# Kernel optimization log

Measured on AMD Instinct MI355X. Metric: run time of the kernel, lower is better.

Reference implementation:

```python
import jax, jax.numpy as jnp
import numpy as np

N = 50000   # nodes
E = 800000  # edges
IN = 128    # input_channels
HID = 256   # hidden_channels
G = 64      # graphs
R = 3       # num_relations
META = 38
EPS = 1e-5


def _glorot(key, shape):
    fan_in, fan_out = shape[-2], shape[-1]
    lim = np.sqrt(6.0 / (fan_in + fan_out)).astype(np.float32)
    return jax.random.uniform(key, shape, jnp.float32, -lim, lim)


def setup_inputs() -> dict:
    key = jax.random.key(0)
    ks = iter(jax.random.split(key, 40))
    inp = {}
    inp["x"] = jax.random.normal(next(ks), (N, IN), jnp.float32)
    inp["edge_attr"] = jax.random.normal(next(ks), (E, 1), jnp.float32)  # unused by module
    inp["edge_index"] = jax.random.randint(next(ks), (2, E), 0, N)
    inp["edge_type"] = jax.random.randint(next(ks), (E,), 0, R)
    inp["MetaData"] = jax.random.normal(next(ks), (G, META), jnp.float32)
    inp["batch"] = jnp.sort(jax.random.randint(next(ks), (N,), 0, G))
    dims = [(IN, 100), (100, HID), (HID, HID), (HID, HID)]
    for l, (din, dout) in enumerate(dims):
        inp[f"W{l}"] = _glorot(next(ks), (R, din, dout))      # per-relation weights
        inp[f"R{l}"] = _glorot(next(ks), (din, dout))          # root weight
        inp[f"b{l}"] = jnp.zeros((dout,), jnp.float32)         # conv bias
        inp[f"g{l}"] = jnp.ones((dout,), jnp.float32)          # BN gamma
        inp[f"bb{l}"] = jnp.zeros((dout,), jnp.float32)        # BN beta
    inp["lin1_w"] = _glorot(next(ks), (HID + META, 100))
    inp["lin1_b"] = jnp.zeros((100,), jnp.float32)
    inp["lin2_w"] = _glorot(next(ks), (100, 1))
    inp["lin2_b"] = jnp.zeros((1,), jnp.float32)
    return inp


def reference(x, edge_attr, edge_index, edge_type, MetaData, batch,
              W0, R0, b0, g0, bb0, W1, R1, b1, g1, bb1,
              W2, R2, b2, g2, bb2, W3, R3, b3, g3, bb3,
              lin1_w, lin1_b, lin2_w, lin2_b):
    src, dst = edge_index[0], edge_index[1]
    seg = edge_type * N + dst  # combined (relation, dst) segment id
    ones_e = jnp.ones((E,), x.dtype)
    cnt = jax.ops.segment_sum(ones_e, seg, num_segments=R * N).reshape(R, N, 1)
    cnt = jnp.maximum(cnt, 1.0)

    def conv(h, W, Rw, b):
        # per-relation transform then gather-scatter mean aggregation (PyG RGCNConv, aggr='mean')
        H = jnp.einsum('ni,rio->rno', h, W)          # [R,N,out]
        msg = H[edge_type, src]                       # [E,out]
        agg = jax.ops.segment_sum(msg, seg, num_segments=R * N)
        agg = agg.reshape(R, N, -1) / cnt
        return agg.sum(0) + h @ Rw + b

    def bn(h, g, bb):  # training-mode BatchNorm1d over nodes
        mu = h.mean(0)
        var = h.var(0)
        return (h - mu) * jax.lax.rsqrt(var + EPS) * g + bb

    for W, Rw, b, g, bb in [(W0, R0, b0, g0, bb0), (W1, R1, b1, g1, bb1),
                            (W2, R2, b2, g2, bb2), (W3, R3, b3, g3, bb3)]:
        x = bn(conv(x, W, Rw, b), g, bb)

    # global_mean_pool
    sums = jax.ops.segment_sum(x, batch, num_segments=G)
    cnts = jax.ops.segment_sum(jnp.ones((N, 1), x.dtype), batch, num_segments=G)
    xg = sums / jnp.maximum(cnts, 1.0)

    h = jnp.concatenate([xg, MetaData], axis=1) @ lin1_w + lin1_b
    # dropout p=0.5 is identity in eval mode
    return h @ lin2_w + lin2_b
```

## Files before the change

kernel.cpp:

```cpp
#include <hip/hip_runtime.h>
#include <hip/hip_bf16.h>

#define NN 50000
#define EE 800000
#define GG 64
#define RR 3
#define METAD 38
#define NSEG (RR*NN)
#define EPSV 1e-5f

typedef __bf16 bf_t;
typedef __attribute__((ext_vector_type(8))) __bf16 bf16x8;
typedef __attribute__((ext_vector_type(4))) __bf16 bf16x4;
typedef __attribute__((ext_vector_type(2))) __bf16 bf16x2;
typedef __attribute__((ext_vector_type(4))) float f32x4;
typedef __attribute__((address_space(1))) void gas_t;
typedef __attribute__((address_space(3))) void las_t;

__device__ __forceinline__ float loadf(const void* p, size_t i, int flag){
  return flag ? ((const float*)p)[i] : (float)(((const bf_t*)p)[i]);
}

__global__ __launch_bounds__(256) void detect_kernel(const void* __restrict__ xraw,
                                                     int* __restrict__ flag){
  __shared__ int found;
  if (threadIdx.x == 0) found = 0;
  __syncthreads();
  const unsigned short* u = (const unsigned short*)xraw;
  for (int i = threadIdx.x; i < 65536; i += 256){
    int e = (u[i] >> 7) & 0xFF;
    if (e >= 0xF0) found = 1;
  }
  __syncthreads();
  if (threadIdx.x == 0) *flag = found;
}

struct CvtJobs {
  const void* src[17];
  float* dst[17];
  int n[17];
};

__global__ __launch_bounds__(256) void cvt_many(CvtJobs j, const int* __restrict__ flag){
  int job = blockIdx.y;
  int i = blockIdx.x*256 + threadIdx.x;
  if (i < j.n[job]) j.dst[job][i] = loadf(j.src[job], i, *flag);
}

__global__ __launch_bounds__(256) void pack_w(const void* __restrict__ W,
                                              const void* __restrict__ R,
                                              bf_t* __restrict__ out,
                                              int D, int O, int dplog,
                                              const int* __restrict__ flag){
  int id = blockIdx.x*256 + threadIdx.x;
  int DP4 = 1 << (dplog + 2);
  int o = id >> (dplog + 2);
  int k = id & (DP4 - 1);
  int r = k >> dplog;
  int i = k & ((1 << dplog) - 1);
  float v = 0.f;
  int fl = *flag;
  if (i < D && o < O){
    if (r < 3) v = loadf(W, ((size_t)r*D + i)*O + o, fl);
    else       v = loadf(R, (size_t)i*O + o, fl);
  }
  out[(size_t)o*DP4 + k] = (bf_t)v;
}

__global__ __launch_bounds__(256) void counti_kernel(const int* __restrict__ ei,
                                                     const int* __restrict__ et,
                                                     int* __restrict__ cnt){
  int e = blockIdx.x*256 + threadIdx.x;
  if (e < EE) atomicAdd(&cnt[et[e]*NN + ei[EE + e]], 1);
}

__global__ __launch_bounds__(256) void rcnt_kernel(const int* __restrict__ cnt,
                                                   float* __restrict__ rcnt){
  int i = blockIdx.x*256 + threadIdx.x;
  if (i < NSEG) rcnt[i] = 1.0f / (float)max(cnt[i], 1);
}

__global__ __launch_bounds__(256) void scan1_kernel(const int* __restrict__ cnt,
                                                    int* __restrict__ segoff,
                                                    int* __restrict__ bsums){
  __shared__ int sh[256];
  int i = blockIdx.x*256 + threadIdx.x;
  int v = (i < NSEG) ? cnt[i] : 0;
  sh[threadIdx.x] = v;
  __syncthreads();
  for (int off = 1; off < 256; off <<= 1){
    int t = 0;
    if (threadIdx.x >= off) t = sh[threadIdx.x - off];
    __syncthreads();
    if (threadIdx.x >= off) sh[threadIdx.x] += t;
    __syncthreads();
  }
  if (i < NSEG) segoff[i] = sh[threadIdx.x] - v;
  if (threadIdx.x == 255) bsums[blockIdx.x] = sh[255];
}

__global__ __launch_bounds__(256) void scan2_kernel(int* __restrict__ bsums, int nb){
  __shared__ int sh[256];
  __shared__ int carry;
  if (threadIdx.x == 0) carry = 0;
  __syncthreads();
  for (int base = 0; base < nb; base += 256){
    int i = base + threadIdx.x;
    int v = (i < nb) ? bsums[i] : 0;
    sh[threadIdx.x] = v;
    __syncthreads();
    for (int off = 1; off < 256; off <<= 1){
      int t = 0;
      if (threadIdx.x >= off) t = sh[threadIdx.x - off];
      __syncthreads();
      if (threadIdx.x >= off) sh[threadIdx.x] += t;
      __syncthreads();
    }
    if (i < nb) bsums[i] = sh[threadIdx.x] - v + carry;
    __syncthreads();
    if (threadIdx.x == 0) carry += sh[255];
    __syncthreads();
  }
}

__global__ __launch_bounds__(256) void scan3_kernel(int* __restrict__ segoff,
                                                    const int* __restrict__ bsums){
  int i = blockIdx.x*256 + threadIdx.x;
  if (i < NSEG) segoff[i] += bsums[blockIdx.x];
  if (i == 0) segoff[NSEG] = EE;
}

__global__ __launch_bounds__(256) void curinit_kernel(const int* __restrict__ segoff,
                                                      int* __restrict__ cursor){
  int i = blockIdx.x*256 + threadIdx.x;
  if (i < NSEG) cursor[i] = segoff[i];
}

__global__ __launch_bounds__(256) void place_kernel(const int* __restrict__ ei,
                                                    const int* __restrict__ et,
                                                    int* __restrict__ cursor,
                                                    int* __restrict__ srcs){
  int e = blockIdx.x*256 + threadIdx.x;
  if (e < EE){
    int seg = et[e]*NN + ei[EE + e];
    int pos = atomicAdd(&cursor[seg], 1);
    srcs[pos] = ei[e];
  }
}

__global__ __launch_bounds__(128) void cvt_x(const void* __restrict__ x,
                                             bf_t* __restrict__ Ab,
                                             const int* __restrict__ flag){
  int d = blockIdx.x, t = threadIdx.x;
  Ab[(size_t)d*512 + 384 + t] = (bf_t)loadf(x, (size_t)d*128 + t, *flag);
}

template<int DP>
__global__ __launch_bounds__(256) void aggregate_wave(const bf_t* __restrict__ Ab, int lda,
                                                      const int* __restrict__ segoff,
                                                      const int* __restrict__ srcs,
                                                      const float* __restrict__ rcnt,
                                                      const bf_t* __restrict__ zrow,
                                                      bf_t* __restrict__ out){
  int wid = (blockIdx.x*256 + threadIdx.x) >> 6;
  if (wid >= NSEG) return;
  wid = __builtin_amdgcn_readfirstlane(wid);
  int lane = threadIdx.x & 63;
  int r = wid / NN;
  int d = wid - r*NN;
  int s0 = segoff[wid], s1 = segoff[wid + 1];
  float rc = rcnt[wid];
  const bf_t* in = Ab + 3*DP;

  if (DP == 256){
    float a0=0.f, a1=0.f, a2=0.f, a3=0.f;
    const int off = lane*4;
    const bf_t* zp = zrow + off;
    int e = s0;
    for (; e + 4 <= s1; e += 4){
      int sA = srcs[e], sB = srcs[e+1], sC = srcs[e+2], sD = srcs[e+3];
      uint2 vA = *(const uint2*)(in + (size_t)sA*lda + off);
      uint2 vB = *(const uint2*)(in + (size_t)sB*lda + off);
      uint2 vC = *(const uint2*)(in + (size_t)sC*lda + off);
      uint2 vD = *(const uint2*)(in + (size_t)sD*lda + off);
      a0 += __uint_as_float(vA.x << 16); a1 += __uint_as_float(vA.x & 0xFFFF0000u);
      a2 += __uint_as_float(vA.y << 16); a3 += __uint_as_float(vA.y & 0xFFFF0000u);
      a0 += __uint_as_float(vB.x << 16); a1 += __uint_as_float(vB.x & 0xFFFF0000u);
      a2 += __uint_as_float(vB.y << 16); a3 += __uint_as_float(vB.y & 0xFFFF0000u);
      a0 += __uint_as_float(vC.x << 16); a1 += __uint_as_float(vC.x & 0xFFFF0000u);
      a2 += __uint_as_float(vC.y << 16); a3 += __uint_as_float(vC.y & 0xFFFF0000u);
      a0 += __uint_as_float(vD.x << 16); a1 += __uint_as_float(vD.x & 0xFFFF0000u);
      a2 += __uint_as_float(vD.y << 16); a3 += __uint_as_float(vD.y & 0xFFFF0000u);
    }
    if (e < s1){
      int sA = srcs[e];
      int sB = srcs[min(e+1, s1-1)];
      int sC = srcs[min(e+2, s1-1)];
      const uint2* pA = (const uint2*)(in + (size_t)sA*lda + off);
      const uint2* pB = (e+1 < s1) ? (const uint2*)(in + (size_t)sB*lda + off) : (const uint2*)zp;
      const uint2* pC = (e+2 < s1) ? (const uint2*)(in + (size_t)sC*lda + off) : (const uint2*)zp;
      uint2 vA = *pA, vB = *pB, vC = *pC;
      a0 += __uint_as_float(vA.x << 16); a1 += __uint_as_float(vA.x & 0xFFFF0000u);
      a2 += __uint_as_float(vA.y << 16); a3 += __uint_as_float(vA.y & 0xFFFF0000u);
      a0 += __uint_as_float(vB.x << 16); a1 += __uint_as_float(vB.x & 0xFFFF0000u);
      a2 += __uint_as_float(vB.y << 16); a3 += __uint_as_float(vB.y & 0xFFFF0000u);
      a0 += __uint_as_float(vC.x << 16); a1 += __uint_as_float(vC.x & 0xFFFF0000u);
      a2 += __uint_as_float(vC.y << 16); a3 += __uint_as_float(vC.y & 0xFFFF0000u);
    }
    bf16x4 o = {(bf_t)(a0*rc), (bf_t)(a1*rc), (bf_t)(a2*rc), (bf_t)(a3*rc)};
    *(bf16x4*)(out + (size_t)d*lda + r*DP + off) = o;
  } else {
    float a0=0.f, a1=0.f;
    const int off = lane*2;
    const bf_t* zp = zrow + off;
    int e = s0;
    for (; e + 4 <= s1; e += 4){
      int sA = srcs[e], sB = srcs[e+1], sC = srcs[e+2], sD = srcs[e+3];
      unsigned vA = *(const unsigned*)(in + (size_t)sA*lda + off);
      unsigned vB = *(const unsigned*)(in + (size_t)sB*lda + off);
      unsigned vC = *(const unsigned*)(in + (size_t)sC*lda + off);
      unsigned vD = *(const unsigned*)(in + (size_t)sD*lda + off);
      a0 += __uint_as_float(vA << 16); a1 += __uint_as_float(vA & 0xFFFF0000u);
      a0 += __uint_as_float(vB << 16); a1 += __uint_as_float(vB & 0xFFFF0000u);
      a0 += __uint_as_float(vC << 16); a1 += __uint_as_float(vC & 0xFFFF0000u);
      a0 += __uint_as_float(vD << 16); a1 += __uint_as_float(vD & 0xFFFF0000u);
    }
    if (e < s1){
      int sA = srcs[e];
      int sB = srcs[min(e+1, s1-1)];
      int sC = srcs[min(e+2, s1-1)];
      const unsigned* pA = (const unsigned*)(in + (size_t)sA*lda + off);
      const unsigned* pB = (e+1 < s1) ? (const unsigned*)(in + (size_t)sB*lda + off) : (const unsigned*)zp;
      const unsigned* pC = (e+2 < s1) ? (const unsigned*)(in + (size_t)sC*lda + off) : (const unsigned*)zp;
      unsigned vA = *pA, vB = *pB, vC = *pC;
      a0 += __uint_as_float(vA << 16); a1 += __uint_as_float(vA & 0xFFFF0000u);
      a0 += __uint_as_float(vB << 16); a1 += __uint_as_float(vB & 0xFFFF0000u);
      a0 += __uint_as_float(vC << 16); a1 += __uint_as_float(vC & 0xFFFF0000u);
    }
    bf16x2 o = {(bf_t)(a0*rc), (bf_t)(a1*rc)};
    *(bf16x2*)(out + (size_t)d*lda + r*DP + off) = o;
  }
}

#define ISSUE2(B_, KO_)                                                                             \
  { uint4* _b = &lds4[B_][0];                                                                       \
    __builtin_amdgcn_global_load_lds((gas_t*)(ArG + (KO_)), (las_t*)(_b + wave*64), 16, 0, 0);      \
    __builtin_amdgcn_global_load_lds((gas_t*)(BrG + (KO_)), (las_t*)(_b + 512 + wave*64), 16, 0, 0); }

template<int NT>
__global__ __launch_bounds__(512) void gemm_mfma2(const bf_t* __restrict__ A, int lda, int K,
                                                  const bf_t* __restrict__ Bt,
                                                  const float* __restrict__ bias,
                                                  float* __restrict__ C, int ldc, int O,
                                                  float* __restrict__ sums){
  constexpr int NI = NT/64;
  __shared__ uint4 lds4[2][1024];
  __shared__ float colsum[2*NT];
  float* stage = (float*)lds4;

  int tid = threadIdx.x;
  int lane = tid & 63;
  int wave = tid >> 6;
  int row0 = blockIdx.x*128;
  int col0 = blockIdx.y*NT;
  int mw = (wave & 1) << 6;
  int nw = (wave >> 1) * (NT/4);
  int l15 = lane & 15, quad = lane >> 4;
  f32x4 acc[4][NI] = {};

  int srow = wave*16 + (lane >> 2);
  int skc8 = (lane & 3) * 8;
  int gra = row0 + srow; if (gra >= NN) gra = NN - 1;
  const bf_t* ArG = A + (size_t)gra*lda + skc8;
  const bf_t* BrG = Bt + (size_t)(col0 + srow)*K + skc8;

  int niter = K >> 5;
  ISSUE2(0, 0)
  ISSUE2(1, 32)

  for (int i = 0; i < niter; ++i){
    if (i + 1 < niter) asm volatile("s_waitcnt vmcnt(2)" ::: "memory");
    else               asm volatile("s_waitcnt vmcnt(0)" ::: "memory");
    __builtin_amdgcn_s_barrier();
    asm volatile("" ::: "memory");
    __builtin_amdgcn_sched_barrier(0);

    const uint4* As4 = &lds4[i & 1][0];
    const uint4* Bs4 = As4 + 512;
    bf16x8 af[4], bfv[NI];
    #pragma unroll
    for (int mi = 0; mi < 4; ++mi){
      int R = mw + mi*16 + l15;
      af[mi] = *(const bf16x8*)&As4[R*4 + quad];
    }
    #pragma unroll
    for (int ni = 0; ni < NI; ++ni){
      int Rb = nw + ni*16 + l15;
      bfv[ni] = *(const bf16x8*)&Bs4[Rb*4 + quad];
    }
    #pragma unroll
    for (int mi = 0; mi < 4; ++mi)
      #pragma unroll
      for (int ni = 0; ni < NI; ++ni)
        acc[mi][ni] = __builtin_amdgcn_mfma_f32_16x16x32_bf16(af[mi], bfv[ni], acc[mi][ni], 0, 0, 0);

    asm volatile("s_waitcnt lgkmcnt(0)" ::: "memory");
    __builtin_amdgcn_s_barrier();
    if (i + 2 < niter) ISSUE2(i & 1, (i + 2) << 5)
  }

  __syncthreads();
  if (tid < 2*NT) colsum[tid] = 0.f;
  float bzv[NI];
  #pragma unroll
  for (int ni = 0; ni < NI; ++ni){
    int col = col0 + nw + ni*16 + l15;
    bzv[ni] = (col < O) ? bias[col] : 0.f;
  }
  __syncthreads();

  #pragma unroll
  for (int ni = 0; ni < NI; ++ni){
    int lcol = nw + ni*16 + l15;
    int col = col0 + lcol;
    if (col < O){
      float scol = 0.f, qcol = 0.f;
      #pragma unroll
      for (int mi = 0; mi < 4; ++mi){
        int rb = row0 + mw + mi*16 + quad*4;
        #pragma unroll
        for (int j = 0; j < 4; ++j){
          if (rb + j < NN){
            float v = acc[mi][ni][j] + bzv[ni];
            scol += v; qcol += v*v;
          }
        }
      }
      atomicAdd(&colsum[lcol], scol);
      atomicAdd(&colsum[NT + lcol], qcol);
    }
  }

  constexpr int STR = NT + 4;
  constexpr int TPR = NT/4;
  constexpr int RPR = 512/TPR;
  int rl0 = tid / TPR;
  int colg = (tid % TPR)*4;
  #pragma unroll
  for (int c = 0; c < 4; ++c){
    __syncthreads();
    if ((wave & 1) == (c >> 1)){
      int base = (c & 1)*32;
      #pragma unroll
      for (int m2 = 0; m2 < 2; ++m2){
        int mi = (base >> 4) + m2;
        #pragma unroll
        for (int ni = 0; ni < NI; ++ni)
          #pragma unroll
          for (int j = 0; j < 4; ++j)
            stage[(mi*16 + quad*4 + j - base)*STR + nw + ni*16 + l15] = acc[mi][ni][j] + bzv[ni];
      }
    }
    __syncthreads();
    #pragma unroll
    for (int p = 0; p < 32/RPR; ++p){
      int rl = p*RPR + rl0;
      int gr = row0 + c*32 + rl;
      if (gr < NN)
        *(float4*)&C[(size_t)gr*ldc + col0 + colg] = *(const float4*)&stage[rl*STR + colg];
    }
  }

  __syncthreads();
  for (int c = tid; c < NT; c += 512){
    int col = col0 + c;
    if (col < O){
      unsafeAtomicAdd(&sums[col], colsum[c]);
      unsafeAtomicAdd(&sums[256 + col], colsum[NT + c]);
    }
  }
}

__global__ __launch_bounds__(256) void bn_finalize(const float* __restrict__ sums,
                                                   const float* __restrict__ g,
                                                   const float* __restrict__ bb,
                                                   float* __restrict__ scale,
                                                   float* __restrict__ shift, int dout){
  int c = threadIdx.x;
  if (c < dout){
    float mu = sums[c] * (1.0f/NN);
    float var = sums[256 + c] * (1.0f/NN) - mu*mu;
    float rstd = rsqrtf(fmaxf(var, 0.f) + EPSV);
    float s = rstd * g[c];
    scale[c] = s;
    shift[c] = bb[c] - mu*s;
  }
}

template<int DPN>
__global__ __launch_bounds__(DPN) void bn_cvt(const float* __restrict__ C, int ldc, int O,
                                              const float* __restrict__ scale,
                                              const float* __restrict__ shift,
                                              bf_t* __restrict__ Ab, int ldan){
  int d = blockIdx.x, t = threadIdx.x;
  float v = 0.f;
  if (t < O) v = C[(size_t)d*ldc + t]*scale[t] + shift[t];
  Ab[(size_t)d*ldan + 3*DPN + t] = (bf_t)v;
}

__device__ __forceinline__ int lower_bound(const int* __restrict__ a, int v){
  int lo = 0, hi = NN;
  while (lo < hi){ int m = (lo+hi) >> 1; if (a[m] < v) lo = m+1; else hi = m; }
  return lo;
}

__global__ __launch_bounds__(256) void pool_kernel(const bf_t* __restrict__ H,
                                                   const int* __restrict__ batch,
                                                   float* __restrict__ pooled){
  int g = blockIdx.x, sl = blockIdx.y;
  int start = lower_bound(batch, g), end = lower_bound(batch, g+1);
  int len = end - start;
  float inv = 1.0f / (float)max(len, 1);
  int chunk = (len + 7) >> 3;
  int s0 = start + sl*chunk;
  int s1 = min(s0 + chunk, end);
  float s = 0.f;
  for (int n = s0; n < s1; ++n) s += (float)H[(size_t)n*1024 + threadIdx.x];
  if (s1 > s0) unsafeAtomicAdd(&pooled[g*256 + threadIdx.x], s * inv);
}

__global__ __launch_bounds__(128) void final_kernel(const float* __restrict__ pooled,
                                                    const float* __restrict__ meta,
                                                    const float* __restrict__ w1,
                                                    const float* __restrict__ b1,
                                                    const float* __restrict__ w2,
                                                    const float* __restrict__ b2,
                                                    void* __restrict__ out,
                                                    const int* __restrict__ flag){
  int g = blockIdx.x;
  __shared__ float h1[100];
  __shared__ float red[128];
  int t = threadIdx.x;
  if (t < 100){
    float acc = b1[t];
    for (int k = 0; k < 256; ++k) acc += pooled[g*256 + k] * w1[k*100 + t];
    for (int k = 0; k < METAD; ++k) acc += meta[g*METAD + k] * w1[(256+k)*100 + t];
    h1[t] = acc;
  }
  __syncthreads();
  red[t] = (t < 100) ? h1[t] * w2[t] : 0.f;
  __syncthreads();
  for (int s = 64; s > 0; s >>= 1){
    if (t < s) red[t] += red[t + s];
    __syncthreads();
  }
  if (t == 0){
    float v = red[0] + b2[0];
    if (*flag) ((float*)out)[g] = v;
    else       ((__hip_bfloat16*)out)[g] = __float2bfloat16(v);
  }
}

extern "C" void kernel_launch(void* const* d_in, const int* in_sizes, int n_in,
                              void* d_out, int out_size, void* d_ws, size_t ws_size,
                              hipStream_t stream){
  const void* x    = d_in[0];
  const int*  ei   = (const int*)d_in[2];
  const int*  et   = (const int*)d_in[3];
  const int*  batch= (const int*)d_in[5];

  float* ws     = (float*)d_ws;
  int*   flag   = (int*)ws;
  float* rcnt   = ws + 16;
  int*   cnt    = (int*)(ws + 150016);
  int*   segoff = (int*)(ws + 300032);
  int*   bsums  = (int*)(ws + 450048);
  int*   srcs   = (int*)(ws + 451072);
  float* sums   = ws + 1251072;
  float* scale  = ws + 1251584;
  float* shift  = ws + 1251840;
  float* pooled = ws + 1252096;
  float* bc     = ws + 1268480;
  float* gc_    = ws + 1269348;
  float* bbc    = ws + 1270216;
  float* metaf  = ws + 1271084;
  float* w1f    = ws + 1273516;
  float* b1f    = ws + 1302916;
  float* w2f    = ws + 1303016;
  float* b2f_   = ws + 1303116;
  bf_t*  wt     = (bf_t*)(ws + 1303168);
  int*   cursor = (int*)(ws + 1663616);
  float* C      = ws + 1813632;
  bf_t*  Ab     = (bf_t*)(ws + 14613632);

  const size_t wtoff[4] = {0, 65536, 196608, 458752};

  detect_kernel<<<1, 256, 0, stream>>>(x, flag);

  const int vsz[4]  = {100, 256, 256, 256};
  const int voff[4] = {0, 100, 356, 612};
  float *bfp[4], *gf[4], *bbf[4];
  CvtJobs J;
  int nj = 0;
  for (int l = 0; l < 4; ++l){
    bfp[l] = bc + voff[l]; gf[l] = gc_ + voff[l]; bbf[l] = bbc + voff[l];
    J.src[nj] = d_in[6 + l*5 + 2]; J.dst[nj] = bfp[l]; J.n[nj] = vsz[l]; nj++;
    J.src[nj] = d_in[6 + l*5 + 3]; J.dst[nj] = gf[l];  J.n[nj] = vsz[l]; nj++;
    J.src[nj] = d_in[6 + l*5 + 4]; J.dst[nj] = bbf[l]; J.n[nj] = vsz[l]; nj++;
  }
  J.src[nj] = d_in[4];  J.dst[nj] = metaf; J.n[nj] = GG*METAD; nj++;
  J.src[nj] = d_in[26]; J.dst[nj] = w1f;   J.n[nj] = 29400; nj++;
  J.src[nj] = d_in[27]; J.dst[nj] = b1f;   J.n[nj] = 100; nj++;
  J.src[nj] = d_in[28]; J.dst[nj] = w2f;   J.n[nj] = 100; nj++;
  J.src[nj] = d_in[29]; J.dst[nj] = b2f_;  J.n[nj] = 1; nj++;
  cvt_many<<<dim3(115, nj), 256, 0, stream>>>(J, flag);

  const int din[4] = {128, 100, 256, 256};
  const int dou[4] = {100, 256, 256, 256};
  const int DP[4]  = {128, 128, 256, 256};
  const int dplog[4] = {7, 7, 8, 8};
  const int Op[4]  = {128, 256, 256, 256};
  for (int l = 0; l < 4; ++l){
    int total = Op[l] << (dplog[l] + 2);
    pack_w<<<total/256, 256, 0, stream>>>(d_in[6 + l*5 + 0], d_in[6 + l*5 + 1],
                                          wt + wtoff[l], din[l], dou[l], dplog[l], flag);
  }

  hipMemsetAsync(cnt, 0, NSEG*sizeof(int), stream);
  counti_kernel<<<(EE+255)/256, 256, 0, stream>>>(ei, et, cnt);
  rcnt_kernel<<<(NSEG+255)/256, 256, 0, stream>>>(cnt, rcnt);
  int nb = (NSEG + 255)/256;
  scan1_kernel<<<nb, 256, 0, stream>>>(cnt, segoff, bsums);
  scan2_kernel<<<1, 256, 0, stream>>>(bsums, nb);
  scan3_kernel<<<nb, 256, 0, stream>>>(segoff, bsums);
  curinit_kernel<<<nb, 256, 0, stream>>>(segoff, cursor);
  place_kernel<<<(EE+255)/256, 256, 0, stream>>>(ei, et, cursor, srcs);
  hipMemsetAsync(bsums, 0, 1024, stream);
  const bf_t* zrow = (const bf_t*)bsums;

  cvt_x<<<NN, 128, 0, stream>>>(x, Ab, flag);

  const int lda[4] = {512, 512, 1024, 1024};
  int aggBlocks = (NSEG + 3)/4;
  for (int l = 0; l < 4; ++l){
    int O = dou[l];
    if (DP[l] == 128)
      aggregate_wave<128><<<aggBlocks, 256, 0, stream>>>(Ab, lda[l], segoff, srcs, rcnt, zrow, Ab);
    else
      aggregate_wave<256><<<aggBlocks, 256, 0, stream>>>(Ab, lda[l], segoff, srcs, rcnt, zrow, Ab);

    hipMemsetAsync(sums, 0, 512*sizeof(float), stream);
    dim3 g2(391, Op[l]/128);
    gemm_mfma2<128><<<g2, 512, 0, stream>>>(Ab, lda[l], 4*DP[l], wt + wtoff[l], bfp[l],
                                            C, Op[l], O, sums);

    bn_finalize<<<1, 256, 0, stream>>>(sums, gf[l], bbf[l], scale, shift, O);

    int DPN = (l < 3) ? DP[l+1] : 256;
    int ldan = (l < 3) ? lda[l+1] : 1024;
    if (DPN == 128)
      bn_cvt<128><<<NN, 128, 0, stream>>>(C, Op[l], O, scale, shift, Ab, ldan);
    else
      bn_cvt<256><<<NN, 256, 0, stream>>>(C, Op[l], O, scale, shift, Ab, ldan);
  }

  hipMemsetAsync(pooled, 0, (size_t)GG*256*sizeof(float), stream);
  pool_kernel<<<dim3(GG, 8), 256, 0, stream>>>(Ab + 768, batch, pooled);
  final_kernel<<<GG, 128, 0, stream>>>(pooled, metaf, w1f, b1f, w2f, b2f_, d_out, flag);
}
```

Measured before the change: 838.2 us.

## Load B fragments straight into registers and XOR-swizzle A tile in LDS

The GEMM kernel stops staging the B (weight) tile through LDS. Each wave now prefetches its own B fragments from global memory into registers one k-step ahead, and only the A tile goes through LDS via global_load_lds. The A tile layout is XOR-swizzled across 16-byte chunks to cut LDS bank conflicts on fragment reads, and the vmcnt waits are adjusted for the extra in-flight register loads. The unrolled MFMA loop hard-codes NI=2 (acc[mi][0..1]), so it is only correct for NT=128. Any other NT instantiation would silently compute wrong results, and B reads are now served by global/L2 rather than shared LDS.

```diff
diff --git a/kernel.cpp b/kernel.cpp
--- a/kernel.cpp
+++ b/kernel.cpp
@@ -242,10 +242,8 @@
   }
 }
 
-#define ISSUE2(B_, KO_)                                                                             \
-  { uint4* _b = &lds4[B_][0];                                                                       \
-    __builtin_amdgcn_global_load_lds((gas_t*)(ArG + (KO_)), (las_t*)(_b + wave*64), 16, 0, 0);      \
-    __builtin_amdgcn_global_load_lds((gas_t*)(BrG + (KO_)), (las_t*)(_b + 512 + wave*64), 16, 0, 0); }
+#define ISSUE_A(B_, KO_)                                                                        \
+  __builtin_amdgcn_global_load_lds((gas_t*)(ArG + (KO_)), (las_t*)(&lds4[B_][0] + wave*64), 16, 0, 0);
 
 template<int NT>
 __global__ __launch_bounds__(512) void gemm_mfma2(const bf_t* __restrict__ A, int lda, int K,
@@ -254,7 +252,7 @@
                                                   float* __restrict__ C, int ldc, int O,
                                                   float* __restrict__ sums){
   constexpr int NI = NT/64;
-  __shared__ uint4 lds4[2][1024];
+  __shared__ uint4 lds4[2][1056];
   __shared__ float colsum[2*NT];
   float* stage = (float*)lds4;
 
@@ -269,44 +267,45 @@
   f32x4 acc[4][NI] = {};
 
   int srow = wave*16 + (lane >> 2);
-  int skc8 = (lane & 3) * 8;
+  int skc8 = ((lane & 3) ^ ((lane >> 3) & 3)) * 8;
   int gra = row0 + srow; if (gra >= NN) gra = NN - 1;
   const bf_t* ArG = A + (size_t)gra*lda + skc8;
-  const bf_t* BrG = Bt + (size_t)(col0 + srow)*K + skc8;
+
+  const bf_t* Bp0 = Bt + (size_t)(col0 + nw + l15)*K + quad*8;
+  const bf_t* Bp1 = Bp0 + (size_t)16*K;
 
   int niter = K >> 5;
-  ISSUE2(0, 0)
-  ISSUE2(1, 32)
+  ISSUE_A(0, 0)
+  bf16x8 bpre0 = *(const bf16x8*)(Bp0);
+  bf16x8 bpre1 = *(const bf16x8*)(Bp1);
+  ISSUE_A(1, 32)
 
   for (int i = 0; i < niter; ++i){
-    if (i + 1 < niter) asm volatile("s_waitcnt vmcnt(2)" ::: "memory");
-    else               asm volatile("s_waitcnt vmcnt(0)" ::: "memory");
+    if (i + 1 < niter) asm volatile("s_waitcnt vmcnt(3)" ::: "memory");
+    else               asm volatile("s_waitcnt vmcnt(2)" ::: "memory");
     __builtin_amdgcn_s_barrier();
     asm volatile("" ::: "memory");
     __builtin_amdgcn_sched_barrier(0);
 
     const uint4* As4 = &lds4[i & 1][0];
-    const uint4* Bs4 = As4 + 512;
-    bf16x8 af[4], bfv[NI];
+    bf16x8 af[4];
     #pragma unroll
     for (int mi = 0; mi < 4; ++mi){
       int R = mw + mi*16 + l15;
-      af[mi] = *(const bf16x8*)&As4[R*4 + quad];
+      af[mi] = *(const bf16x8*)&As4[R*4 + (quad ^ ((R >> 1) & 3))];
     }
     #pragma unroll
-    for (int ni = 0; ni < NI; ++ni){
-      int Rb = nw + ni*16 + l15;
-      bfv[ni] = *(const bf16x8*)&Bs4[Rb*4 + quad];
-    }
-    #pragma unroll
-    for (int mi = 0; mi < 4; ++mi)
-      #pragma unroll
-      for (int ni = 0; ni < NI; ++ni)
-        acc[mi][ni] = __builtin_amdgcn_mfma_f32_16x16x32_bf16(af[mi], bfv[ni], acc[mi][ni], 0, 0, 0);
-
+    for (int mi = 0; mi < 4; ++mi){
+      acc[mi][0] = __builtin_amdgcn_mfma_f32_16x16x32_bf16(af[mi], bpre0, acc[mi][0], 0, 0, 0);
+      acc[mi][1] = __builtin_amdgcn_mfma_f32_16x16x32_bf16(af[mi], bpre1, acc[mi][1], 0, 0, 0);
+    }
+    if (i + 1 < niter){
+      bpre0 = *(const bf16x8*)(Bp0 + ((i + 1) << 5));
+      bpre1 = *(const bf16x8*)(Bp1 + ((i + 1) << 5));
+    }
     asm volatile("s_waitcnt lgkmcnt(0)" ::: "memory");
     __builtin_amdgcn_s_barrier();
-    if (i + 2 < niter) ISSUE2(i & 1, (i + 2) << 5)
+    if (i + 2 < niter) ISSUE_A(i & 1, (i + 2) << 5)
   }
 
   __syncthreads();
```

New measurement: 925.6 us. 10.4% more time.
